# Kernel tuning notes

Hardware: AMD Instinct MI355X
Metric: run time of the kernel (lower is better)

## Reference

```python
import jax, jax.numpy as jnp
import numpy as np

D_MODEL = 1024
NUM_HEADS = 8
D_HEAD = D_MODEL // NUM_HEADS
EPS = 1e-5


def layer_norm(x, gamma, beta):
    mu = jnp.mean(x, axis=-1, keepdims=True)
    var = jnp.mean((x - mu) ** 2, axis=-1, keepdims=True)
    return (x - mu) * jax.lax.rsqrt(var + EPS) * gamma + beta


def setup_inputs() -> dict:
    key = jax.random.key(0)
    ks = jax.random.split(key, 16)
    B, N, M, D = 4, 1024, 1024, D_MODEL
    s = 0.02
    inp = {
        "input_states": jax.random.normal(ks[0], (B, N, D), jnp.float32),
        "memory_states": jax.random.normal(ks[1], (B, M, D), jnp.float32),
        "memory_weights": jax.random.uniform(ks[2], (B, M), jnp.float32),
        "memory_masks": jax.random.randint(ks[3], (B, M), 0, 2).astype(bool),
        "attention_factors": jax.random.uniform(ks[4], (B, N, M), jnp.float32),
        "attention_masks": jax.random.randint(ks[5], (B, 1, N, M), 0, 2).astype(bool),
        "Wq": jax.random.normal(ks[6], (D, D), jnp.float32) * s,
        "bq": jnp.zeros((D,), jnp.float32),
        "Wk": jax.random.normal(ks[7], (D, D), jnp.float32) * s,
        "bk": jnp.zeros((D,), jnp.float32),
        "Wv": jax.random.normal(ks[8], (D, D), jnp.float32) * s,
        "bv": jnp.zeros((D,), jnp.float32),
        "Wo": jax.random.normal(ks[9], (D, D), jnp.float32) * s,
        "bo": jnp.zeros((D,), jnp.float32),
        "g1": jnp.ones((D,), jnp.float32),
        "b1": jnp.zeros((D,), jnp.float32),
        "We": jax.random.normal(ks[10], (2 * D, D), jnp.float32) * s,
        "be": jnp.zeros((2 * D,), jnp.float32),
        "Ws": jax.random.normal(ks[11], (D, 2 * D), jnp.float32) * s,
        "bs": jnp.zeros((D,), jnp.float32),
        "g2": jnp.ones((D,), jnp.float32),
        "b2": jnp.zeros((D,), jnp.float32),
    }
    return inp


def reference(input_states, memory_states, memory_weights, memory_masks,
              attention_factors, attention_masks,
              Wq, bq, Wk, bk, Wv, bv, Wo, bo, g1, b1,
              We, be, Ws, bs, g2, b2):
    B, N, D = input_states.shape
    M = memory_states.shape[1]
    H, C = NUM_HEADS, D_HEAD
    # QKV projections, split heads: (B, H, len, C)
    q = (input_states @ Wq.T + bq).reshape(B, N, H, C).transpose(0, 2, 1, 3)
    k = (memory_states @ Wk.T + bk).reshape(B, M, H, C).transpose(0, 2, 1, 3)
    v = (memory_states @ Wv.T + bv).reshape(B, M, H, C).transpose(0, 2, 1, 3)
    scores = jnp.einsum('bhnc,bhmc->bhnm', q, k) / jnp.sqrt(jnp.float32(C))
    scores = attention_factors[:, None, :, :] * scores
    scores = scores * memory_weights[:, None, None, :]
    neg_inf = jnp.float32(-jnp.inf)
    scores = jnp.where(memory_masks[:, None, None, :], neg_inf, scores)
    scores = jnp.where(attention_masks, neg_inf, scores)
    attn = jax.nn.softmax(scores, axis=-1)  # (B,H,N,M)
    hidden = jnp.einsum('bhnm,bhmc->bhnc', attn, v)
    hidden = hidden.transpose(0, 2, 1, 3).reshape(B, N, D)
    hidden = hidden @ Wo.T + bo
    out1 = layer_norm(hidden + input_states, g1, b1)
    # FFN: expand -> ReLU -> squeeze -> residual + LN
    h = jax.nn.relu(out1 @ We.T + be)
    h = h @ Ws.T + bs
    out = layer_norm(out1 + h, g2, b2)
    return out, attn
```

## Files before the change

kernel.cpp:

```cpp
#include <hip/hip_runtime.h>
#include <hip/hip_bf16.h>

typedef __bf16 bf16_t;
typedef __bf16 bf16x4 __attribute__((ext_vector_type(4)));
typedef __bf16 bf16x8 __attribute__((ext_vector_type(8)));
typedef float f32x4 __attribute__((ext_vector_type(4)));

typedef const __attribute__((address_space(1))) void gvoid_t;
typedef __attribute__((address_space(3))) void lvoid_t;

#define MB (1UL<<20)

__device__ __forceinline__ void gload_lds16(const void* g, void* l) {
    __builtin_amdgcn_global_load_lds((gvoid_t*)g, (lvoid_t*)l, 16, 0, 0);
}

__global__ __launch_bounds__(256) void cast_kernel(const float* __restrict__ in,
                                                   bf16_t* __restrict__ out, int n4) {
    int i = blockIdx.x * 256 + threadIdx.x;
    if (i < n4) {
        float4 f = ((const float4*)in)[i];
        bf16x4 o;
        o[0] = (bf16_t)f.x; o[1] = (bf16_t)f.y; o[2] = (bf16_t)f.z; o[3] = (bf16_t)f.w;
        ((bf16x4*)out)[i] = o;
    }
}

template<int A_F32, int OUT_BF16, int HAS_BIAS, int RELU, int HAS_RES, int VT_OUT>
__global__ __launch_bounds__(256)
void gemm_bt(const void* __restrict__ Ap, int lda,
             const bf16_t* __restrict__ Bp, int ldb,
             const float* __restrict__ bias,
             const float* __restrict__ res, int ldres,
             void* __restrict__ Cp, int ldc,
             int K, int tilesN,
             long sAb, long sAh, long sBb, long sBh, long sCb, long sCh,
             int nH)
{
    __shared__ bf16_t sA[128 * 32];
    __shared__ bf16_t sB[128 * 32];

    const int z = blockIdx.y;
    const int bb = z / nH, hh = z % nH;
    const int tile = blockIdx.x;
    const int tm = tile / tilesN, tn = tile % tilesN;
    const int rowBase = tm * 128, colBase = tn * 128;
    const int t = threadIdx.x;
    const int wave = t >> 6, lane = t & 63;
    const int wr = (wave >> 1) * 64, wc = (wave & 1) * 64;

    const bf16_t* Bbase = Bp + (long)bb * sBb + (long)hh * sBh;

    f32x4 acc[4][4] = {};

    const int e0 = t * 8;
    const int r0row = e0 >> 5, scol = e0 & 31;
    const int r1row = r0row + 64;

    for (int k0 = 0; k0 < K; k0 += 32) {
        if constexpr (A_F32) {
            const float* Af = (const float*)Ap + (long)bb * sAb + (long)hh * sAh;
            #pragma unroll
            for (int r = 0; r < 2; ++r) {
                const int row = r ? r1row : r0row;
                const float* src = Af + (long)(rowBase + row) * lda + k0 + scol;
                float4 f0 = *(const float4*)src;
                float4 f1 = *(const float4*)(src + 4);
                bf16x8 v;
                v[0] = (bf16_t)f0.x; v[1] = (bf16_t)f0.y; v[2] = (bf16_t)f0.z; v[3] = (bf16_t)f0.w;
                v[4] = (bf16_t)f1.x; v[5] = (bf16_t)f1.y; v[6] = (bf16_t)f1.z; v[7] = (bf16_t)f1.w;
                *(bf16x8*)&sA[r * 2048 + e0] = v;
            }
        } else {
            const bf16_t* Ab = (const bf16_t*)Ap + (long)bb * sAb + (long)hh * sAh;
            #pragma unroll
            for (int r = 0; r < 2; ++r) {
                const int row = r ? r1row : r0row;
                const bf16_t* src = Ab + (long)(rowBase + row) * lda + k0 + scol;
                char* dst = (char*)sA + r * 4096 + wave * 1024;
                gload_lds16(src, dst);
            }
        }
        #pragma unroll
        for (int r = 0; r < 2; ++r) {
            const int row = r ? r1row : r0row;
            const bf16_t* src = Bbase + (long)(colBase + row) * ldb + k0 + scol;
            char* dst = (char*)sB + r * 4096 + wave * 1024;
            gload_lds16(src, dst);
        }
        asm volatile("s_waitcnt vmcnt(0)" ::: "memory");
        __syncthreads();

        const int kf = (lane >> 4) * 8;
        const int lr = lane & 15;
        bf16x8 af[4], bfr[4];
        #pragma unroll
        for (int m = 0; m < 4; ++m) af[m] = *(const bf16x8*)&sA[(wr + m * 16 + lr) * 32 + kf];
        #pragma unroll
        for (int n = 0; n < 4; ++n) bfr[n] = *(const bf16x8*)&sB[(wc + n * 16 + lr) * 32 + kf];
        #pragma unroll
        for (int m = 0; m < 4; ++m)
            #pragma unroll
            for (int n = 0; n < 4; ++n)
                acc[m][n] = __builtin_amdgcn_mfma_f32_16x16x32_bf16(af[m], bfr[n], acc[m][n], 0, 0, 0);
        __syncthreads();
    }

    const long cOff = (long)bb * sCb + (long)hh * sCh;
    #pragma unroll
    for (int m = 0; m < 4; ++m) {
        #pragma unroll
        for (int r = 0; r < 4; ++r) {
            const int i = rowBase + wr + m * 16 + (lane >> 4) * 4 + r;
            #pragma unroll
            for (int n = 0; n < 4; ++n) {
                const int j = colBase + wc + n * 16 + (lane & 15);
                float v = acc[m][n][r];
                if constexpr (HAS_BIAS) v += bias[j];
                if constexpr (RELU) v = fmaxf(v, 0.0f);
                if constexpr (HAS_RES) v += res[(long)i * ldres + j];
                if constexpr (VT_OUT) {
                    const long o = (((long)(i >> 10) * 8 + (j >> 7)) * 128 + (j & 127)) * 1024 + (i & 1023);
                    ((bf16_t*)Cp)[o] = (bf16_t)v;
                } else if constexpr (OUT_BF16) {
                    ((bf16_t*)Cp)[cOff + (long)i * ldc + j] = (bf16_t)v;
                } else {
                    ((float*)Cp)[cOff + (long)i * ldc + j] = v;
                }
            }
        }
    }
}

__global__ __launch_bounds__(256)
void softmax_kernel(float* __restrict__ attn,
                    const float* __restrict__ factors,
                    const float* __restrict__ weights,
                    const int* __restrict__ mmask,
                    const int* __restrict__ amask)
{
    const int row = blockIdx.x * 4 + (threadIdx.x >> 6);
    const int lane = threadIdx.x & 63;
    const int n = row & 1023;
    const int b = row >> 13;
    float* p = attn + (long)row * 1024;
    const float4* fac = (const float4*)(factors + ((long)b * 1024 + n) * 1024);
    const float4* wt  = (const float4*)(weights + (long)b * 1024);
    const int4*   mm  = (const int4*)(mmask + (long)b * 1024);
    const int4*   am  = (const int4*)(amask + ((long)b * 1024 + n) * 1024);
    const float scale = 0.08838834764831845f;
    const float NEGINF = -__builtin_inff();

    float vals[16];
    float mx = NEGINF;
    #pragma unroll
    for (int jj = 0; jj < 4; ++jj) {
        const int v4 = lane + jj * 64;
        float4 sc = ((const float4*)p)[v4];
        float4 fa = fac[v4];
        float4 w4 = wt[v4];
        int4 m4 = mm[v4];
        int4 a4 = am[v4];
        float s0 = sc.x * scale * fa.x * w4.x; if (m4.x | a4.x) s0 = NEGINF;
        float s1 = sc.y * scale * fa.y * w4.y; if (m4.y | a4.y) s1 = NEGINF;
        float s2 = sc.z * scale * fa.z * w4.z; if (m4.z | a4.z) s2 = NEGINF;
        float s3 = sc.w * scale * fa.w * w4.w; if (m4.w | a4.w) s3 = NEGINF;
        vals[jj * 4 + 0] = s0; vals[jj * 4 + 1] = s1;
        vals[jj * 4 + 2] = s2; vals[jj * 4 + 3] = s3;
        mx = fmaxf(mx, fmaxf(fmaxf(s0, s1), fmaxf(s2, s3)));
    }
    #pragma unroll
    for (int off = 32; off > 0; off >>= 1) mx = fmaxf(mx, __shfl_xor(mx, off));
    float sum = 0.f;
    #pragma unroll
    for (int q = 0; q < 16; ++q) { float e = __expf(vals[q] - mx); vals[q] = e; sum += e; }
    #pragma unroll
    for (int off = 32; off > 0; off >>= 1) sum += __shfl_xor(sum, off);
    const float inv = 1.0f / sum;
    #pragma unroll
    for (int jj = 0; jj < 4; ++jj) {
        const int v4 = lane + jj * 64;
        float4 o;
        o.x = vals[jj * 4 + 0] * inv; o.y = vals[jj * 4 + 1] * inv;
        o.z = vals[jj * 4 + 2] * inv; o.w = vals[jj * 4 + 3] * inv;
        ((float4*)p)[v4] = o;
    }
}

template<int WRITE_BF16>
__global__ __launch_bounds__(256)
void ln_kernel(const float* __restrict__ x,
               const float* __restrict__ g,
               const float* __restrict__ bt,
               float* __restrict__ outf,
               bf16_t* __restrict__ outb)
{
    const int row = blockIdx.x * 4 + (threadIdx.x >> 6);
    const int lane = threadIdx.x & 63;
    const float* p = x + (long)row * 1024;
    float v[16];
    float s = 0.f;
    #pragma unroll
    for (int jj = 0; jj < 4; ++jj) {
        float4 f = ((const float4*)p)[lane + jj * 64];
        v[jj * 4 + 0] = f.x; v[jj * 4 + 1] = f.y; v[jj * 4 + 2] = f.z; v[jj * 4 + 3] = f.w;
        s += f.x + f.y + f.z + f.w;
    }
    #pragma unroll
    for (int off = 32; off > 0; off >>= 1) s += __shfl_xor(s, off);
    const float mu = s * (1.0f / 1024.0f);
    float q = 0.f;
    #pragma unroll
    for (int i = 0; i < 16; ++i) { float d = v[i] - mu; q += d * d; }
    #pragma unroll
    for (int off = 32; off > 0; off >>= 1) q += __shfl_xor(q, off);
    const float rstd = rsqrtf(q * (1.0f / 1024.0f) + 1e-5f);
    #pragma unroll
    for (int jj = 0; jj < 4; ++jj) {
        const int v4 = lane + jj * 64;
        float4 gg = ((const float4*)g)[v4];
        float4 bb = ((const float4*)bt)[v4];
        float4 o;
        o.x = (v[jj * 4 + 0] - mu) * rstd * gg.x + bb.x;
        o.y = (v[jj * 4 + 1] - mu) * rstd * gg.y + bb.y;
        o.z = (v[jj * 4 + 2] - mu) * rstd * gg.z + bb.z;
        o.w = (v[jj * 4 + 3] - mu) * rstd * gg.w + bb.w;
        ((float4*)outf)[(long)row * 256 + v4] = o;
        if constexpr (WRITE_BF16) {
            bf16x4 ob;
            ob[0] = (bf16_t)o.x; ob[1] = (bf16_t)o.y; ob[2] = (bf16_t)o.z; ob[3] = (bf16_t)o.w;
            ((bf16x4*)outb)[(long)row * 256 + v4] = ob;
        }
    }
}

extern "C" void kernel_launch(void* const* d_in, const int* in_sizes, int n_in,
                              void* d_out, int out_size, void* d_ws, size_t ws_size,
                              hipStream_t stream)
{
    (void)in_sizes; (void)n_in; (void)out_size; (void)ws_size;
    const float* input_states     = (const float*)d_in[0];
    const float* memory_states    = (const float*)d_in[1];
    const float* memory_weights   = (const float*)d_in[2];
    const int*   memory_masks     = (const int*)d_in[3];
    const float* attention_factors= (const float*)d_in[4];
    const int*   attention_masks  = (const int*)d_in[5];
    const float* Wq = (const float*)d_in[6];
    const float* bq = (const float*)d_in[7];
    const float* Wk = (const float*)d_in[8];
    const float* bk = (const float*)d_in[9];
    const float* Wv = (const float*)d_in[10];
    const float* bv = (const float*)d_in[11];
    const float* Wo = (const float*)d_in[12];
    const float* bo = (const float*)d_in[13];
    const float* g1 = (const float*)d_in[14];
    const float* b1 = (const float*)d_in[15];
    const float* We = (const float*)d_in[16];
    const float* be = (const float*)d_in[17];
    const float* Ws = (const float*)d_in[18];
    const float* bs = (const float*)d_in[19];
    const float* g2 = (const float*)d_in[20];
    const float* b2 = (const float*)d_in[21];

    float* out0 = (float*)d_out;
    float* attn = (float*)d_out + 4L * 1024 * 1024;

    char* ws = (char*)d_ws;
    bf16_t* Wqb  = (bf16_t*)(ws + 0 * MB);
    bf16_t* Wkb  = (bf16_t*)(ws + 2 * MB);
    bf16_t* Wvb  = (bf16_t*)(ws + 4 * MB);
    bf16_t* Wob  = (bf16_t*)(ws + 6 * MB);
    bf16_t* Web  = (bf16_t*)(ws + 8 * MB);
    bf16_t* Wsb  = (bf16_t*)(ws + 12 * MB);
    bf16_t* inb  = (bf16_t*)(ws + 16 * MB);
    bf16_t* memb = (bf16_t*)(ws + 24 * MB);
    bf16_t* Qb   = (bf16_t*)(ws + 32 * MB);
    bf16_t* Kb   = (bf16_t*)(ws + 40 * MB);
    bf16_t* Vtb  = (bf16_t*)(ws + 48 * MB);
    bf16_t* hidb = (bf16_t*)(ws + 56 * MB);
    float*  preLN= (float*)(ws + 64 * MB);
    float*  out1f= (float*)(ws + 80 * MB);
    bf16_t* out1b= (bf16_t*)(ws + 96 * MB);
    bf16_t* hffn = (bf16_t*)(ws + 104 * MB);

    auto cast = [&](const float* src, bf16_t* dst, long n) {
        cast_kernel<<<(int)(n / 4 / 256), 256, 0, stream>>>(src, dst, (int)(n / 4));
    };
    cast(Wq, Wqb, 1024L * 1024);
    cast(Wk, Wkb, 1024L * 1024);
    cast(Wv, Wvb, 1024L * 1024);
    cast(Wo, Wob, 1024L * 1024);
    cast(We, Web, 2048L * 1024);
    cast(Ws, Wsb, 1024L * 2048);
    cast(input_states, inb, 4096L * 1024);
    cast(memory_states, memb, 4096L * 1024);

    gemm_bt<0,1,1,0,0,0><<<dim3(256, 1), 256, 0, stream>>>(
        inb, 1024, Wqb, 1024, bq, nullptr, 0, Qb, 1024, 1024, 8, 0,0,0,0,0,0, 1);
    gemm_bt<0,1,1,0,0,0><<<dim3(256, 1), 256, 0, stream>>>(
        memb, 1024, Wkb, 1024, bk, nullptr, 0, Kb, 1024, 1024, 8, 0,0,0,0,0,0, 1);
    gemm_bt<0,1,1,0,0,1><<<dim3(256, 1), 256, 0, stream>>>(
        memb, 1024, Wvb, 1024, bv, nullptr, 0, Vtb, 1024, 1024, 8, 0,0,0,0,0,0, 1);
    gemm_bt<0,0,0,0,0,0><<<dim3(64, 32), 256, 0, stream>>>(
        Qb, 1024, Kb, 1024, nullptr, nullptr, 0, attn, 1024, 128, 8,
        1048576L, 128L, 1048576L, 128L, 8388608L, 1048576L, 8);
    softmax_kernel<<<8192, 256, 0, stream>>>(attn, attention_factors, memory_weights,
                                             memory_masks, attention_masks);
    gemm_bt<1,1,0,0,0,0><<<dim3(8, 32), 256, 0, stream>>>(
        attn, 1024, Vtb, 1024, nullptr, nullptr, 0, hidb, 1024, 1024, 1,
        8388608L, 1048576L, 1048576L, 131072L, 1048576L, 128L, 8);
    gemm_bt<0,0,1,0,1,0><<<dim3(256, 1), 256, 0, stream>>>(
        hidb, 1024, Wob, 1024, bo, input_states, 1024, preLN, 1024, 1024, 8, 0,0,0,0,0,0, 1);
    ln_kernel<1><<<1024, 256, 0, stream>>>(preLN, g1, b1, out1f, out1b);
    gemm_bt<0,1,1,1,0,0><<<dim3(512, 1), 256, 0, stream>>>(
        out1b, 1024, Web, 1024, be, nullptr, 0, hffn, 2048, 1024, 16, 0,0,0,0,0,0, 1);
    gemm_bt<0,0,1,0,1,0><<<dim3(256, 1), 256, 0, stream>>>(
        hffn, 2048, Wsb, 2048, bs, out1f, 1024, preLN, 1024, 2048, 8, 0,0,0,0,0,0, 1);
    ln_kernel<0><<<1024, 256, 0, stream>>>(preLN, g2, b2, out0, nullptr);
}
```

Baseline: 397.5 us.

## Fuse QK^T, masked softmax and PV into one attention kernel

Replaces the separate score GEMM, softmax pass, and attn@V GEMM with a single kernel. Each block handles 16 query rows for one batch-head: it computes the scores with MFMA, applies the scale, factors, weights and masks, runs the softmax in LDS, writes the fp32 attention map, and multiplies the bf16 probabilities by V^T straight from shared memory. This removes the fp32 score round-trip to global memory and the fp32 re-read and bf16 cast of attention in the PV GEMM. In exchange, K and V are read from global memory without LDS staging or reuse across blocks, the block uses 64KB of LDS, and the factor and mask reads are scalar.

Result: slower. 411.6 us (+3.6%).

```diff
diff --git a/kernel.cpp b/kernel.cpp
--- a/kernel.cpp
+++ b/kernel.cpp
@@ -26,22 +26,18 @@
     }
 }
 
-template<int A_F32, int OUT_BF16, int HAS_BIAS, int RELU, int HAS_RES, int VT_OUT>
+template<int OUT_BF16, int HAS_BIAS, int RELU, int HAS_RES, int VT_OUT>
 __global__ __launch_bounds__(256)
-void gemm_bt(const void* __restrict__ Ap, int lda,
+void gemm_bt(const bf16_t* __restrict__ Ap, int lda,
              const bf16_t* __restrict__ Bp, int ldb,
              const float* __restrict__ bias,
              const float* __restrict__ res, int ldres,
              void* __restrict__ Cp, int ldc,
-             int K, int tilesN,
-             long sAb, long sAh, long sBb, long sBh, long sCb, long sCh,
-             int nH)
+             int K, int tilesN)
 {
     __shared__ bf16_t sA[128 * 32];
     __shared__ bf16_t sB[128 * 32];
 
-    const int z = blockIdx.y;
-    const int bb = z / nH, hh = z % nH;
     const int tile = blockIdx.x;
     const int tm = tile / tilesN, tn = tile % tilesN;
     const int rowBase = tm * 128, colBase = tn * 128;
@@ -49,8 +45,6 @@
     const int wave = t >> 6, lane = t & 63;
     const int wr = (wave >> 1) * 64, wc = (wave & 1) * 64;
 
-    const bf16_t* Bbase = Bp + (long)bb * sBb + (long)hh * sBh;
-
     f32x4 acc[4][4] = {};
 
     const int e0 = t * 8;
@@ -58,35 +52,15 @@
     const int r1row = r0row + 64;
 
     for (int k0 = 0; k0 < K; k0 += 32) {
-        if constexpr (A_F32) {
-            const float* Af = (const float*)Ap + (long)bb * sAb + (long)hh * sAh;
-            #pragma unroll
-            for (int r = 0; r < 2; ++r) {
-                const int row = r ? r1row : r0row;
-                const float* src = Af + (long)(rowBase + row) * lda + k0 + scol;
-                float4 f0 = *(const float4*)src;
-                float4 f1 = *(const float4*)(src + 4);
-                bf16x8 v;
-                v[0] = (bf16_t)f0.x; v[1] = (bf16_t)f0.y; v[2] = (bf16_t)f0.z; v[3] = (bf16_t)f0.w;
-                v[4] = (bf16_t)f1.x; v[5] = (bf16_t)f1.y; v[6] = (bf16_t)f1.z; v[7] = (bf16_t)f1.w;
-                *(bf16x8*)&sA[r * 2048 + e0] = v;
-            }
-        } else {
-            const bf16_t* Ab = (const bf16_t*)Ap + (long)bb * sAb + (long)hh * sAh;
-            #pragma unroll
-            for (int r = 0; r < 2; ++r) {
-                const int row = r ? r1row : r0row;
-                const bf16_t* src = Ab + (long)(rowBase + row) * lda + k0 + scol;
-                char* dst = (char*)sA + r * 4096 + wave * 1024;
-                gload_lds16(src, dst);
-            }
-        }
         #pragma unroll
         for (int r = 0; r < 2; ++r) {
             const int row = r ? r1row : r0row;
-            const bf16_t* src = Bbase + (long)(colBase + row) * ldb + k0 + scol;
-            char* dst = (char*)sB + r * 4096 + wave * 1024;
-            gload_lds16(src, dst);
+            const bf16_t* srcA = Ap + (long)(rowBase + row) * lda + k0 + scol;
+            char* dstA = (char*)sA + r * 4096 + wave * 1024;
+            gload_lds16(srcA, dstA);
+            const bf16_t* srcB = Bp + (long)(colBase + row) * ldb + k0 + scol;
+            char* dstB = (char*)sB + r * 4096 + wave * 1024;
+            gload_lds16(srcB, dstB);
         }
         asm volatile("s_waitcnt vmcnt(0)" ::: "memory");
         __syncthreads();
@@ -106,7 +80,6 @@
         __syncthreads();
     }
 
-    const long cOff = (long)bb * sCb + (long)hh * sCh;
     #pragma unroll
     for (int m = 0; m < 4; ++m) {
         #pragma unroll
@@ -123,68 +96,109 @@
                     const long o = (((long)(i >> 10) * 8 + (j >> 7)) * 128 + (j & 127)) * 1024 + (i & 1023);
                     ((bf16_t*)Cp)[o] = (bf16_t)v;
                 } else if constexpr (OUT_BF16) {
-                    ((bf16_t*)Cp)[cOff + (long)i * ldc + j] = (bf16_t)v;
+                    ((bf16_t*)Cp)[(long)i * ldc + j] = (bf16_t)v;
                 } else {
-                    ((float*)Cp)[cOff + (long)i * ldc + j] = v;
+                    ((float*)Cp)[(long)i * ldc + j] = v;
                 }
             }
         }
     }
 }
 
-__global__ __launch_bounds__(256)
-void softmax_kernel(float* __restrict__ attn,
-                    const float* __restrict__ factors,
-                    const float* __restrict__ weights,
-                    const int* __restrict__ mmask,
-                    const int* __restrict__ amask)
+__global__ __launch_bounds__(512)
+void fused_attn_kernel(const bf16_t* __restrict__ Qb,
+                       const bf16_t* __restrict__ Kb,
+                       const bf16_t* __restrict__ Vtb,
+                       const float* __restrict__ factors,
+                       const float* __restrict__ weights,
+                       const int* __restrict__ mmask,
+                       const int* __restrict__ amask,
+                       float* __restrict__ attn,
+                       bf16_t* __restrict__ hidb)
 {
-    const int row = blockIdx.x * 4 + (threadIdx.x >> 6);
-    const int lane = threadIdx.x & 63;
-    const int n = row & 1023;
-    const int b = row >> 13;
-    float* p = attn + (long)row * 1024;
-    const float4* fac = (const float4*)(factors + ((long)b * 1024 + n) * 1024);
-    const float4* wt  = (const float4*)(weights + (long)b * 1024);
-    const int4*   mm  = (const int4*)(mmask + (long)b * 1024);
-    const int4*   am  = (const int4*)(amask + ((long)b * 1024 + n) * 1024);
+    __shared__ float sS[16 * 1024];
+    const int bh = blockIdx.y;
+    const int b = bh >> 3, h = bh & 7;
+    const int n0 = blockIdx.x * 16;
+    const int t = threadIdx.x, wave = t >> 6, lane = t & 63;
+    const int lr = lane & 15, lk = lane >> 4;
     const float scale = 0.08838834764831845f;
     const float NEGINF = -__builtin_inff();
 
-    float vals[16];
-    float mx = NEGINF;
-    #pragma unroll
-    for (int jj = 0; jj < 4; ++jj) {
-        const int v4 = lane + jj * 64;
-        float4 sc = ((const float4*)p)[v4];
-        float4 fa = fac[v4];
-        float4 w4 = wt[v4];
-        int4 m4 = mm[v4];
-        int4 a4 = am[v4];
-        float s0 = sc.x * scale * fa.x * w4.x; if (m4.x | a4.x) s0 = NEGINF;
-        float s1 = sc.y * scale * fa.y * w4.y; if (m4.y | a4.y) s1 = NEGINF;
-        float s2 = sc.z * scale * fa.z * w4.z; if (m4.z | a4.z) s2 = NEGINF;
-        float s3 = sc.w * scale * fa.w * w4.w; if (m4.w | a4.w) s3 = NEGINF;
-        vals[jj * 4 + 0] = s0; vals[jj * 4 + 1] = s1;
-        vals[jj * 4 + 2] = s2; vals[jj * 4 + 3] = s3;
-        mx = fmaxf(mx, fmaxf(fmaxf(s0, s1), fmaxf(s2, s3)));
-    }
-    #pragma unroll
-    for (int off = 32; off > 0; off >>= 1) mx = fmaxf(mx, __shfl_xor(mx, off));
-    float sum = 0.f;
-    #pragma unroll
-    for (int q = 0; q < 16; ++q) { float e = __expf(vals[q] - mx); vals[q] = e; sum += e; }
-    #pragma unroll
-    for (int off = 32; off > 0; off >>= 1) sum += __shfl_xor(sum, off);
-    const float inv = 1.0f / sum;
-    #pragma unroll
-    for (int jj = 0; jj < 4; ++jj) {
-        const int v4 = lane + jj * 64;
-        float4 o;
-        o.x = vals[jj * 4 + 0] * inv; o.y = vals[jj * 4 + 1] * inv;
-        o.z = vals[jj * 4 + 2] * inv; o.w = vals[jj * 4 + 3] * inv;
-        ((float4*)p)[v4] = o;
-    }
+    const bf16_t* Qp = Qb + ((long)b * 1024 + n0) * 1024 + h * 128;
+    bf16x8 aq[4];
+    #pragma unroll
+    for (int kk = 0; kk < 4; ++kk)
+        aq[kk] = *(const bf16x8*)(Qp + (long)lr * 1024 + kk * 32 + lk * 8);
+
+    const bf16_t* Kp = Kb + (long)b * 1024 * 1024 + h * 128;
+
+    for (int mt = 0; mt < 8; ++mt) {
+        const int c0 = mt * 128 + wave * 16;
+        f32x4 acc = {};
+        #pragma unroll
+        for (int kk = 0; kk < 4; ++kk) {
+            bf16x8 bk = *(const bf16x8*)(Kp + (long)(c0 + lr) * 1024 + kk * 32 + lk * 8);
+            acc = __builtin_amdgcn_mfma_f32_16x16x32_bf16(aq[kk], bk, acc, 0, 0, 0);
+        }
+        const int colm = c0 + lr;
+        const float w = weights[b * 1024 + colm];
+        const int mm = mmask[b * 1024 + colm];
+        #pragma unroll
+        for (int r = 0; r < 4; ++r) {
+            const int row = lk * 4 + r;
+            const long fi = ((long)b * 1024 + n0 + row) * 1024 + colm;
+            float s = acc[r] * scale * factors[fi] * w;
+            if (mm | amask[fi]) s = NEGINF;
+            sS[row * 1024 + (colm ^ ((row & 7) << 2))] = s;
+        }
+    }
+    __syncthreads();
+
+    #pragma unroll
+    for (int rr = 0; rr < 2; ++rr) {
+        const int row = wave * 2 + rr;
+        float vals[16];
+        float mx = NEGINF;
+        #pragma unroll
+        for (int q = 0; q < 16; ++q) {
+            const int c = lane + q * 64;
+            float v = sS[row * 1024 + (c ^ ((row & 7) << 2))];
+            vals[q] = v; mx = fmaxf(mx, v);
+        }
+        #pragma unroll
+        for (int off = 32; off; off >>= 1) mx = fmaxf(mx, __shfl_xor(mx, off));
+        float sum = 0.f;
+        #pragma unroll
+        for (int q = 0; q < 16; ++q) { float e = __expf(vals[q] - mx); vals[q] = e; sum += e; }
+        #pragma unroll
+        for (int off = 32; off; off >>= 1) sum += __shfl_xor(sum, off);
+        const float inv = 1.0f / sum;
+        float* arow = attn + ((long)bh * 1024 + n0 + row) * 1024;
+        #pragma unroll
+        for (int q = 0; q < 16; ++q) {
+            const int c = lane + q * 64;
+            const float p = vals[q] * inv;
+            arow[c] = p;
+            const int byt = (row * 4096 + c * 2) ^ ((row & 7) << 4);
+            *(bf16_t*)((char*)sS + byt) = (bf16_t)p;
+        }
+    }
+    __syncthreads();
+
+    f32x4 o = {};
+    const bf16_t* Vp = Vtb + ((long)bh * 128 + wave * 16 + lr) * 1024;
+    for (int m0 = 0; m0 < 1024; m0 += 32) {
+        const int k0 = m0 + lk * 8;
+        const int byt = (lr * 4096 + k0 * 2) ^ ((lr & 7) << 4);
+        bf16x8 pa = *(const bf16x8*)((const char*)sS + byt);
+        bf16x8 vb = *(const bf16x8*)(Vp + k0);
+        o = __builtin_amdgcn_mfma_f32_16x16x32_bf16(pa, vb, o, 0, 0, 0);
+    }
+    bf16_t* hp = hidb + ((long)b * 1024 + n0) * 1024 + h * 128 + wave * 16;
+    #pragma unroll
+    for (int r = 0; r < 4; ++r)
+        hp[(long)(lk * 4 + r) * 1024 + lr] = (bf16_t)o[r];
 }
 
 template<int WRITE_BF16>
@@ -295,26 +309,21 @@
     cast(input_states, inb, 4096L * 1024);
     cast(memory_states, memb, 4096L * 1024);
 
-    gemm_bt<0,1,1,0,0,0><<<dim3(256, 1), 256, 0, stream>>>(
-        inb, 1024, Wqb, 1024, bq, nullptr, 0, Qb, 1024, 1024, 8, 0,0,0,0,0,0, 1);
-    gemm_bt<0,1,1,0,0,0><<<dim3(256, 1), 256, 0, stream>>>(
-        memb, 1024, Wkb, 1024, bk, nullptr, 0, Kb, 1024, 1024, 8, 0,0,0,0,0,0, 1);
-    gemm_bt<0,1,1,0,0,1><<<dim3(256, 1), 256, 0, stream>>>(
-        memb, 1024, Wvb, 1024, bv, nullptr, 0, Vtb, 1024, 1024, 8, 0,0,0,0,0,0, 1);
-    gemm_bt<0,0,0,0,0,0><<<dim3(64, 32), 256, 0, stream>>>(
-        Qb, 1024, Kb, 1024, nullptr, nullptr, 0, attn, 1024, 128, 8,
-        1048576L, 128L, 1048576L, 128L, 8388608L, 1048576L, 8);
-    softmax_kernel<<<8192, 256, 0, stream>>>(attn, attention_factors, memory_weights,
-                                             memory_masks, attention_masks);
-    gemm_bt<1,1,0,0,0,0><<<dim3(8, 32), 256, 0, stream>>>(
-        attn, 1024, Vtb, 1024, nullptr, nullptr, 0, hidb, 1024, 1024, 1,
-        8388608L, 1048576L, 1048576L, 131072L, 1048576L, 128L, 8);
-    gemm_bt<0,0,1,0,1,0><<<dim3(256, 1), 256, 0, stream>>>(
-        hidb, 1024, Wob, 1024, bo, input_states, 1024, preLN, 1024, 1024, 8, 0,0,0,0,0,0, 1);
+    gemm_bt<1,1,0,0,0><<<dim3(256), 256, 0, stream>>>(
+        inb, 1024, Wqb, 1024, bq, nullptr, 0, Qb, 1024, 1024, 8);
+    gemm_bt<1,1,0,0,0><<<dim3(256), 256, 0, stream>>>(
+        memb, 1024, Wkb, 1024, bk, nullptr, 0, Kb, 1024, 1024, 8);
+    gemm_bt<1,1,0,0,1><<<dim3(256), 256, 0, stream>>>(
+        memb, 1024, Wvb, 1024, bv, nullptr, 0, Vtb, 1024, 1024, 8);
+    fused_attn_kernel<<<dim3(64, 32), 512, 0, stream>>>(
+        Qb, Kb, Vtb, attention_factors, memory_weights, memory_masks,
+        attention_masks, attn, hidb);
+    gemm_bt<0,1,0,1,0><<<dim3(256), 256, 0, stream>>>(
+        hidb, 1024, Wob, 1024, bo, input_states, 1024, preLN, 1024, 1024, 8);
     ln_kernel<1><<<1024, 256, 0, stream>>>(preLN, g1, b1, out1f, out1b);
-    gemm_bt<0,1,1,1,0,0><<<dim3(512, 1), 256, 0, stream>>>(
-        out1b, 1024, Web, 1024, be, nullptr, 0, hffn, 2048, 1024, 16, 0,0,0,0,0,0, 1);
-    gemm_bt<0,0,1,0,1,0><<<dim3(256, 1), 256, 0, stream>>>(
-        hffn, 2048, Wsb, 2048, bs, out1f, 1024, preLN, 1024, 2048, 8, 0,0,0,0,0,0, 1);
+    gemm_bt<1,1,1,0,0><<<dim3(512), 256, 0, stream>>>(
+        out1b, 1024, Web, 1024, be, nullptr, 0, hffn, 2048, 1024, 16);
+    gemm_bt<0,1,0,1,0><<<dim3(256), 256, 0, stream>>>(
+        hffn, 2048, Wsb, 2048, bs, out1f, 1024, preLN, 1024, 2048, 8);
     ln_kernel<0><<<1024, 256, 0, stream>>>(preLN, g2, b2, out0, nullptr);
 }
```

## Fuse softmax normalization into PV GEMM using precomputed row stats

Applied to the files above, without the earlier changes.

Splits softmax into a stats kernel that only computes the row max and inverse sum, and a PV kernel. The PV kernel recomputes the masked, scaled scores, writes the normalized attention probabilities, and feeds them as bf16 straight into the MFMA. This drops one full read/write pass over the 128MB fp32 attention tensor. In exchange the PV kernel re-reads factors and masks per tile, and its global loads for the A operand are synchronous and not overlapped.

Result: slower. 416.8 us (+4.9%).

```diff
diff --git a/kernel.cpp b/kernel.cpp
--- a/kernel.cpp
+++ b/kernel.cpp
@@ -26,22 +26,25 @@
     }
 }
 
-template<int A_F32, int OUT_BF16, int HAS_BIAS, int RELU, int HAS_RES, int VT_OUT>
+template<int OUT_BF16, int HAS_BIAS, int RELU, int HAS_RES, int VT_OUT>
 __global__ __launch_bounds__(256)
-void gemm_bt(const void* __restrict__ Ap, int lda,
+void gemm_bt(const bf16_t* __restrict__ Ap, int lda,
              const bf16_t* __restrict__ Bp, int ldb,
              const float* __restrict__ bias,
              const float* __restrict__ res, int ldres,
              void* __restrict__ Cp, int ldc,
              int K, int tilesN,
-             long sAb, long sAh, long sBb, long sBh, long sCb, long sCh,
-             int nH)
+             long aOffB, long aOffH, long bOffB, long bOffH, long cOffZ, int nH)
 {
     __shared__ bf16_t sA[128 * 32];
     __shared__ bf16_t sB[128 * 32];
 
     const int z = blockIdx.y;
-    const int bb = z / nH, hh = z % nH;
+    const int zb = z / nH, zh = z % nH;
+    Ap += zb * aOffB + zh * aOffH;
+    Bp += zb * bOffB + zh * bOffH;
+    const long cOff = (long)z * cOffZ;
+
     const int tile = blockIdx.x;
     const int tm = tile / tilesN, tn = tile % tilesN;
     const int rowBase = tm * 128, colBase = tn * 128;
@@ -49,8 +52,6 @@
     const int wave = t >> 6, lane = t & 63;
     const int wr = (wave >> 1) * 64, wc = (wave & 1) * 64;
 
-    const bf16_t* Bbase = Bp + (long)bb * sBb + (long)hh * sBh;
-
     f32x4 acc[4][4] = {};
 
     const int e0 = t * 8;
@@ -58,35 +59,15 @@
     const int r1row = r0row + 64;
 
     for (int k0 = 0; k0 < K; k0 += 32) {
-        if constexpr (A_F32) {
-            const float* Af = (const float*)Ap + (long)bb * sAb + (long)hh * sAh;
-            #pragma unroll
-            for (int r = 0; r < 2; ++r) {
-                const int row = r ? r1row : r0row;
-                const float* src = Af + (long)(rowBase + row) * lda + k0 + scol;
-                float4 f0 = *(const float4*)src;
-                float4 f1 = *(const float4*)(src + 4);
-                bf16x8 v;
-                v[0] = (bf16_t)f0.x; v[1] = (bf16_t)f0.y; v[2] = (bf16_t)f0.z; v[3] = (bf16_t)f0.w;
-                v[4] = (bf16_t)f1.x; v[5] = (bf16_t)f1.y; v[6] = (bf16_t)f1.z; v[7] = (bf16_t)f1.w;
-                *(bf16x8*)&sA[r * 2048 + e0] = v;
-            }
-        } else {
-            const bf16_t* Ab = (const bf16_t*)Ap + (long)bb * sAb + (long)hh * sAh;
-            #pragma unroll
-            for (int r = 0; r < 2; ++r) {
-                const int row = r ? r1row : r0row;
-                const bf16_t* src = Ab + (long)(rowBase + row) * lda + k0 + scol;
-                char* dst = (char*)sA + r * 4096 + wave * 1024;
-                gload_lds16(src, dst);
-            }
-        }
         #pragma unroll
         for (int r = 0; r < 2; ++r) {
             const int row = r ? r1row : r0row;
-            const bf16_t* src = Bbase + (long)(colBase + row) * ldb + k0 + scol;
-            char* dst = (char*)sB + r * 4096 + wave * 1024;
-            gload_lds16(src, dst);
+            const bf16_t* srcA = Ap + (long)(rowBase + row) * lda + k0 + scol;
+            char* dstA = (char*)sA + r * 4096 + wave * 1024;
+            gload_lds16(srcA, dstA);
+            const bf16_t* srcB = Bp + (long)(colBase + row) * ldb + k0 + scol;
+            char* dstB = (char*)sB + r * 4096 + wave * 1024;
+            gload_lds16(srcB, dstB);
         }
         asm volatile("s_waitcnt vmcnt(0)" ::: "memory");
         __syncthreads();
@@ -106,7 +87,6 @@
         __syncthreads();
     }
 
-    const long cOff = (long)bb * sCb + (long)hh * sCh;
     #pragma unroll
     for (int m = 0; m < 4; ++m) {
         #pragma unroll
@@ -133,17 +113,18 @@
 }
 
 __global__ __launch_bounds__(256)
-void softmax_kernel(float* __restrict__ attn,
-                    const float* __restrict__ factors,
-                    const float* __restrict__ weights,
-                    const int* __restrict__ mmask,
-                    const int* __restrict__ amask)
+void stats_kernel(const float* __restrict__ Sraw,
+                  const float* __restrict__ factors,
+                  const float* __restrict__ weights,
+                  const int* __restrict__ mmask,
+                  const int* __restrict__ amask,
+                  float2* __restrict__ stats)
 {
     const int row = blockIdx.x * 4 + (threadIdx.x >> 6);
     const int lane = threadIdx.x & 63;
     const int n = row & 1023;
     const int b = row >> 13;
-    float* p = attn + (long)row * 1024;
+    const float* p = Sraw + (long)row * 1024;
     const float4* fac = (const float4*)(factors + ((long)b * 1024 + n) * 1024);
     const float4* wt  = (const float4*)(weights + (long)b * 1024);
     const int4*   mm  = (const int4*)(mmask + (long)b * 1024);
@@ -173,17 +154,127 @@
     for (int off = 32; off > 0; off >>= 1) mx = fmaxf(mx, __shfl_xor(mx, off));
     float sum = 0.f;
     #pragma unroll
-    for (int q = 0; q < 16; ++q) { float e = __expf(vals[q] - mx); vals[q] = e; sum += e; }
+    for (int q = 0; q < 16; ++q) sum += __expf(vals[q] - mx);
     #pragma unroll
     for (int off = 32; off > 0; off >>= 1) sum += __shfl_xor(sum, off);
-    const float inv = 1.0f / sum;
-    #pragma unroll
-    for (int jj = 0; jj < 4; ++jj) {
-        const int v4 = lane + jj * 64;
-        float4 o;
-        o.x = vals[jj * 4 + 0] * inv; o.y = vals[jj * 4 + 1] * inv;
-        o.z = vals[jj * 4 + 2] * inv; o.w = vals[jj * 4 + 3] * inv;
-        ((float4*)p)[v4] = o;
+    if (lane == 0) {
+        float2 o; o.x = mx; o.y = 1.0f / sum;
+        stats[row] = o;
+    }
+}
+
+__global__ __launch_bounds__(256)
+void pv_kernel(float* __restrict__ Sio,
+               const bf16_t* __restrict__ Vtb,
+               const float* __restrict__ factors,
+               const float* __restrict__ weights,
+               const int* __restrict__ mmask,
+               const int* __restrict__ amask,
+               const float2* __restrict__ stats,
+               bf16_t* __restrict__ hidb)
+{
+    __shared__ bf16_t sA[128 * 32];
+    __shared__ bf16_t sB[128 * 32];
+
+    const int bh = blockIdx.y;
+    const int b = bh >> 3, h = bh & 7;
+    const int rowBase = blockIdx.x * 128;
+    const int t = threadIdx.x;
+    const int wave = t >> 6, lane = t & 63;
+    const int wr = (wave >> 1) * 64, wc = (wave & 1) * 64;
+    const float scale = 0.08838834764831845f;
+    const float NEGINF = -__builtin_inff();
+
+    float* Sp = Sio + (long)bh * 1048576;
+    const bf16_t* Bp = Vtb + (long)bh * 131072;
+
+    f32x4 acc[4][4] = {};
+
+    const int e0 = t * 8;
+    const int r0row = e0 >> 5, scol = e0 & 31;
+    const int r1row = r0row + 64;
+
+    for (int k0 = 0; k0 < 1024; k0 += 32) {
+        #pragma unroll
+        for (int r = 0; r < 2; ++r) {
+            const int row = r ? r1row : r0row;
+            const bf16_t* srcB = Bp + (long)row * 1024 + k0 + scol;
+            gload_lds16(srcB, (char*)sB + r * 4096 + wave * 1024);
+        }
+        #pragma unroll
+        for (int r = 0; r < 2; ++r) {
+            const int row = r ? r1row : r0row;
+            const int i = rowBase + row;
+            float* srow = Sp + (long)i * 1024 + k0 + scol;
+            float4 s0 = *(const float4*)srow;
+            float4 s1 = *(const float4*)(srow + 4);
+            const float* frow = factors + ((long)b * 1024 + i) * 1024 + k0 + scol;
+            float4 f0 = *(const float4*)frow;
+            float4 f1 = *(const float4*)(frow + 4);
+            const int* arow = amask + ((long)b * 1024 + i) * 1024 + k0 + scol;
+            int4 a0 = *(const int4*)arow;
+            int4 a1 = *(const int4*)(arow + 4);
+            const float* wrow = weights + b * 1024 + k0 + scol;
+            float4 w0 = *(const float4*)wrow;
+            float4 w1 = *(const float4*)(wrow + 4);
+            const int* mrow = mmask + b * 1024 + k0 + scol;
+            int4 m0 = *(const int4*)mrow;
+            int4 m1 = *(const int4*)(mrow + 4);
+            float2 ML = stats[(long)bh * 1024 + i];
+
+            float sg[8];
+            sg[0] = (m0.x | a0.x) ? NEGINF : s0.x * scale * f0.x * w0.x;
+            sg[1] = (m0.y | a0.y) ? NEGINF : s0.y * scale * f0.y * w0.y;
+            sg[2] = (m0.z | a0.z) ? NEGINF : s0.z * scale * f0.z * w0.z;
+            sg[3] = (m0.w | a0.w) ? NEGINF : s0.w * scale * f0.w * w0.w;
+            sg[4] = (m1.x | a1.x) ? NEGINF : s1.x * scale * f1.x * w1.x;
+            sg[5] = (m1.y | a1.y) ? NEGINF : s1.y * scale * f1.y * w1.y;
+            sg[6] = (m1.z | a1.z) ? NEGINF : s1.z * scale * f1.z * w1.z;
+            sg[7] = (m1.w | a1.w) ? NEGINF : s1.w * scale * f1.w * w1.w;
+
+            float p[8];
+            bf16x8 pb;
+            #pragma unroll
+            for (int q = 0; q < 8; ++q) {
+                p[q] = __expf(sg[q] - ML.x) * ML.y;
+                pb[q] = (bf16_t)p[q];
+            }
+            float4 o0, o1;
+            o0.x = p[0]; o0.y = p[1]; o0.z = p[2]; o0.w = p[3];
+            o1.x = p[4]; o1.y = p[5]; o1.z = p[6]; o1.w = p[7];
+            *(float4*)srow = o0;
+            *(float4*)(srow + 4) = o1;
+            *(bf16x8*)&sA[r * 2048 + e0] = pb;
+        }
+        asm volatile("s_waitcnt vmcnt(0)" ::: "memory");
+        __syncthreads();
+
+        const int kf = (lane >> 4) * 8;
+        const int lr = lane & 15;
+        bf16x8 af[4], bfr[4];
+        #pragma unroll
+        for (int m = 0; m < 4; ++m) af[m] = *(const bf16x8*)&sA[(wr + m * 16 + lr) * 32 + kf];
+        #pragma unroll
+        for (int n = 0; n < 4; ++n) bfr[n] = *(const bf16x8*)&sB[(wc + n * 16 + lr) * 32 + kf];
+        #pragma unroll
+        for (int m = 0; m < 4; ++m)
+            #pragma unroll
+            for (int n = 0; n < 4; ++n)
+                acc[m][n] = __builtin_amdgcn_mfma_f32_16x16x32_bf16(af[m], bfr[n], acc[m][n], 0, 0, 0);
+        __syncthreads();
+    }
+
+    #pragma unroll
+    for (int m = 0; m < 4; ++m) {
+        #pragma unroll
+        for (int r = 0; r < 4; ++r) {
+            const int i = rowBase + wr + m * 16 + (lane >> 4) * 4 + r;
+            #pragma unroll
+            for (int n = 0; n < 4; ++n) {
+                const int j = wc + n * 16 + (lane & 15);
+                hidb[((long)b * 1024 + i) * 1024 + h * 128 + j] = (bf16_t)acc[m][n][r];
+            }
+        }
     }
 }
 
@@ -282,6 +373,7 @@
     float*  out1f= (float*)(ws + 80 * MB);
     bf16_t* out1b= (bf16_t*)(ws + 96 * MB);
     bf16_t* hffn = (bf16_t*)(ws + 104 * MB);
+    float2* stats= (float2*)(ws + 112 * MB);
 
     auto cast = [&](const float* src, bf16_t* dst, long n) {
         cast_kernel<<<(int)(n / 4 / 256), 256, 0, stream>>>(src, dst, (int)(n / 4));
@@ -295,26 +387,26 @@
     cast(input_states, inb, 4096L * 1024);
     cast(memory_states, memb, 4096L * 1024);
 
-    gemm_bt<0,1,1,0,0,0><<<dim3(256, 1), 256, 0, stream>>>(
-        inb, 1024, Wqb, 1024, bq, nullptr, 0, Qb, 1024, 1024, 8, 0,0,0,0,0,0, 1);
-    gemm_bt<0,1,1,0,0,0><<<dim3(256, 1), 256, 0, stream>>>(
-        memb, 1024, Wkb, 1024, bk, nullptr, 0, Kb, 1024, 1024, 8, 0,0,0,0,0,0, 1);
-    gemm_bt<0,1,1,0,0,1><<<dim3(256, 1), 256, 0, stream>>>(
-        memb, 1024, Wvb, 1024, bv, nullptr, 0, Vtb, 1024, 1024, 8, 0,0,0,0,0,0, 1);
-    gemm_bt<0,0,0,0,0,0><<<dim3(64, 32), 256, 0, stream>>>(
+    gemm_bt<1,1,0,0,0><<<dim3(256, 1), 256, 0, stream>>>(
+        inb, 1024, Wqb, 1024, bq, nullptr, 0, Qb, 1024, 1024, 8, 0,0,0,0,0, 1);
+    gemm_bt<1,1,0,0,0><<<dim3(256, 1), 256, 0, stream>>>(
+        memb, 1024, Wkb, 1024, bk, nullptr, 0, Kb, 1024, 1024, 8, 0,0,0,0,0, 1);
+    gemm_bt<1,1,0,0,1><<<dim3(256, 1), 256, 0, stream>>>(
+        memb, 1024, Wvb, 1024, bv, nullptr, 0, Vtb, 1024, 1024, 8, 0,0,0,0,0, 1);
+    gemm_bt<0,0,0,0,0><<<dim3(64, 32), 256, 0, stream>>>(
         Qb, 1024, Kb, 1024, nullptr, nullptr, 0, attn, 1024, 128, 8,
-        1048576L, 128L, 1048576L, 128L, 8388608L, 1048576L, 8);
-    softmax_kernel<<<8192, 256, 0, stream>>>(attn, attention_factors, memory_weights,
-                                             memory_masks, attention_masks);
-    gemm_bt<1,1,0,0,0,0><<<dim3(8, 32), 256, 0, stream>>>(
-        attn, 1024, Vtb, 1024, nullptr, nullptr, 0, hidb, 1024, 1024, 1,
-        8388608L, 1048576L, 1048576L, 131072L, 1048576L, 128L, 8);
-    gemm_bt<0,0,1,0,1,0><<<dim3(256, 1), 256, 0, stream>>>(
-        hidb, 1024, Wob, 1024, bo, input_states, 1024, preLN, 1024, 1024, 8, 0,0,0,0,0,0, 1);
+        1048576L, 128L, 1048576L, 128L, 1048576L, 8);
+    stats_kernel<<<8192, 256, 0, stream>>>(attn, attention_factors, memory_weights,
+                                           memory_masks, attention_masks, stats);
+    pv_kernel<<<dim3(8, 32), 256, 0, stream>>>(attn, Vtb, attention_factors,
+                                               memory_weights, memory_masks,
+                                               attention_masks, stats, hidb);
+    gemm_bt<0,1,0,1,0><<<dim3(256, 1), 256, 0, stream>>>(
+        hidb, 1024, Wob, 1024, bo, input_states, 1024, preLN, 1024, 1024, 8, 0,0,0,0,0, 1);
     ln_kernel<1><<<1024, 256, 0, stream>>>(preLN, g1, b1, out1f, out1b);
-    gemm_bt<0,1,1,1,0,0><<<dim3(512, 1), 256, 0, stream>>>(
-        out1b, 1024, Web, 1024, be, nullptr, 0, hffn, 2048, 1024, 16, 0,0,0,0,0,0, 1);
-    gemm_bt<0,0,1,0,1,0><<<dim3(256, 1), 256, 0, stream>>>(
-        hffn, 2048, Wsb, 2048, bs, out1f, 1024, preLN, 1024, 2048, 8, 0,0,0,0,0,0, 1);
+    gemm_bt<1,1,1,0,0><<<dim3(512, 1), 256, 0, stream>>>(
+        out1b, 1024, Web, 1024, be, nullptr, 0, hffn, 2048, 1024, 16, 0,0,0,0,0, 1);
+    gemm_bt<0,1,0,1,0><<<dim3(256, 1), 256, 0, stream>>>(
+        hffn, 2048, Wsb, 2048, bs, out1f, 1024, preLN, 1024, 2048, 8, 0,0,0,0,0, 1);
     ln_kernel<0><<<1024, 256, 0, stream>>>(preLN, g2, b2, out0, nullptr);
 }
```
